# Kernel optimization log

Measured on AMD Instinct MI355X. Metric: run time of the kernel, lower is better.

The kernel has to match this reference:

```python
import jax, jax.numpy as jnp
import numpy as np

N = 50000          # nodes
E = 1_600_000      # edges (avg degree 32)
IN_DIM = 1024
HID = 32           # int(sqrt(IN_DIM))
OUT_DIMS = (2, 3)  # multi-task classifier heads


def setup_inputs() -> dict:
    key = jax.random.key(0)
    ks = jax.random.split(key, 16)
    x = jax.random.normal(ks[0], (N, IN_DIM), dtype=jnp.float32)
    adj_rows = jax.random.randint(ks[1], (E,), 0, N, dtype=jnp.int32)
    adj_cols = jax.random.randint(ks[2], (E,), 0, N, dtype=jnp.int32)
    adj_vals = jax.random.uniform(ks[3], (E,), dtype=jnp.float32) / 32.0  # ~normalized adj

    def xn(k, fan_in, fan_out, gain=0.75):  # xavier_normal with gain 3/4 (selu_xn)
        std = gain * np.sqrt(2.0 / (fan_in + fan_out))
        return jax.random.normal(k, (fan_in, fan_out), dtype=jnp.float32) * std

    w1 = xn(ks[4], IN_DIM, HID)
    w2 = xn(ks[5], HID, HID)
    w3 = xn(ks[6], HID, HID)
    b1 = jnp.zeros((HID,), jnp.float32)
    b2 = jnp.zeros((HID,), jnp.float32)
    b3 = jnp.zeros((HID,), jnp.float32)
    # clf heads: nn.Linear(HID, num_class), xavier_normal gain 1, zero bias
    clf_w0 = xn(ks[7], HID, OUT_DIMS[0], gain=1.0).T  # stored torch-style [out, in]
    clf_w1 = xn(ks[8], HID, OUT_DIMS[1], gain=1.0).T
    clf_b0 = jnp.zeros((OUT_DIMS[0],), jnp.float32)
    clf_b1 = jnp.zeros((OUT_DIMS[1],), jnp.float32)
    return {"x": x, "adj_rows": adj_rows, "adj_cols": adj_cols, "adj_vals": adj_vals,
            "w1": w1, "b1": b1, "w2": w2, "b2": b2, "w3": w3, "b3": b3,
            "clf_w0": clf_w0, "clf_b0": clf_b0, "clf_w1": clf_w1, "clf_b1": clf_b1}


def reference(x, adj_rows, adj_cols, adj_vals, w1, b1, w2, b2, w3, b3,
              clf_w0, clf_b0, clf_w1, clf_b1):
    def gcn_layer(h, w, b):
        support = h @ w                                   # [N, out]
        msgs = adj_vals[:, None] * support[adj_cols]      # gather along edges
        agg = jax.ops.segment_sum(msgs, adj_rows, num_segments=N)  # SpMM
        # eval mode: UniformDropout is identity; then SELU, then bias add
        return jax.nn.selu(agg) + b

    h = gcn_layer(x, w1, b1)
    h = gcn_layer(h, w2, b2)
    h = gcn_layer(h, w3, b3)
    out0 = h @ clf_w0.T + clf_b0   # [N, 2]
    out1 = h @ clf_w1.T + clf_b1   # [N, 3]
    return (out0, out1)
```

## Files before the change

### kernel.cpp

```cpp
#include <hip/hip_runtime.h>

#define IN_DIM 1024
#define HID 32
#define BSHIFT 5
#define BROWS 32
#define MAXB 1600
#define NBLK 128
#define SORT_CAP 4096

typedef _Float16 h4 __attribute__((ext_vector_type(4)));

__device__ __forceinline__ float4 h4_to_f4(h4 v) {
    float4 r;
    r.x = (float)v.x; r.y = (float)v.y; r.z = (float)v.z; r.w = (float)v.w;
    return r;
}

__device__ __forceinline__ float selu_f(float x) {
    const float scale = 1.0507009873554805f;
    const float alpha = 1.6732632423543772f;
    return x > 0.f ? scale * x : scale * alpha * (expf(x) - 1.f);
}


__global__ __launch_bounds__(1024) void part_hist(const int* __restrict__ rows, int E, int NB,
                                                  int nchunk, int* __restrict__ counts) {
    __shared__ int lh[MAXB];
    int tid = threadIdx.x, blk = blockIdx.x;
    for (int b = tid; b < NB; b += 1024) lh[b] = 0;
    __syncthreads();
    int base = blk * nchunk;
    int end = base + nchunk; if (end > E) end = E;
    for (int i = base + tid; i < end; i += 1024)
        atomicAdd(&lh[rows[i] >> BSHIFT], 1);
    __syncthreads();
    for (int b = tid; b < NB; b += 1024) counts[blk * NB + b] = lh[b];
}

__global__ __launch_bounds__(1024) void scan1_kernel(const int* __restrict__ counts, int M,
                                                     int NB,
                                                     int* __restrict__ offs,
                                                     int* __restrict__ partials) {
    __shared__ int s[1024];
    int tid = threadIdx.x;
    int i = blockIdx.x * 1024 + tid;
    int v = 0;
    if (i < M) {
        int b = i >> 7;
        int blk = i & (NBLK - 1);
        v = counts[blk * NB + b];
    }
    s[tid] = v;
    __syncthreads();
    for (int off = 1; off < 1024; off <<= 1) {
        int t = (tid >= off) ? s[tid - off] : 0;
        __syncthreads();
        s[tid] += t;
        __syncthreads();
    }
    if (i < M) offs[i] = s[tid] - v;
    if (tid == 1023) partials[blockIdx.x] = s[tid];
}

__global__ __launch_bounds__(1024) void scan_fix_kernel(int* __restrict__ offs,
                                                        const int* __restrict__ partials,
                                                        int M, int nb1) {
    __shared__ int s[256];
    int tid = threadIdx.x;
    if (tid < 256) s[tid] = (tid < nb1) ? partials[tid] : 0;
    __syncthreads();
    for (int off = 1; off < 256; off <<= 1) {
        int t = 0;
        if (tid < 256 && tid >= off) t = s[tid - off];
        __syncthreads();
        if (tid < 256) s[tid] += t;
        __syncthreads();
    }
    int myoff = (blockIdx.x == 0) ? 0 : s[blockIdx.x - 1];
    int i = blockIdx.x * 1024 + tid;
    if (i < M) offs[i] += myoff;
}

__global__ __launch_bounds__(1024) void part_scatter(const int* __restrict__ rows,
                                                     const int* __restrict__ cols,
                                                     const float* __restrict__ vals, int E,
                                                     int NB, int nchunk,
                                                     const int* __restrict__ offs,
                                                     int2* __restrict__ edata) {
    __shared__ int lc[MAXB];
    int tid = threadIdx.x, blk = blockIdx.x;
    for (int b = tid; b < NB; b += 1024) lc[b] = offs[b * NBLK + blk];
    __syncthreads();
    int base = blk * nchunk;
    int end = base + nchunk; if (end > E) end = E;
    for (int i = base + tid; i < end; i += 1024) {
        int r = rows[i];
        int b = r >> BSHIFT;
        int p = atomicAdd(&lc[b], 1);
        int2 pr;
        pr.x = ((r & (BROWS - 1)) << 18) | cols[i];
        pr.y = __float_as_int(vals[i]);
        edata[p] = pr;
    }
}

__global__ __launch_bounds__(256) void bucket_sort(int2* __restrict__ edata,
                                                   const int* __restrict__ offs,
                                                   int E, int NB,
                                                   int* __restrict__ rowptr) {
    __shared__ int2 stage[SORT_CAP];
    __shared__ int cnt[32], startsh[32], cur[32];
    int b = blockIdx.x, tid = threadIdx.x;
    int s0 = offs[b * NBLK];
    int s1 = (b + 1 < NB) ? offs[(b + 1) * NBLK] : E;
    int n = s1 - s0;
    if (tid < 32) cnt[tid] = 0;
    __syncthreads();
    for (int i = tid; i < n; i += 256) {
        int2 pr = edata[s0 + i];
        stage[i] = pr;
        atomicAdd(&cnt[pr.x >> 18], 1);
    }
    __syncthreads();
    if (tid == 0) {
        int run = 0;
        #pragma unroll
        for (int k = 0; k < 32; ++k) { startsh[k] = run; run += cnt[k]; }
    }
    __syncthreads();
    if (tid < 32) {
        cur[tid] = startsh[tid];
        rowptr[b * BROWS + tid] = s0 + startsh[tid];
    }
    __syncthreads();
    for (int i = tid; i < n; i += 256) {
        int2 pr = stage[i];
        int p = atomicAdd(&cur[pr.x >> 18], 1);
        edata[s0 + p] = pr;
    }
}


#define BR 128
#define BK 64
#define XS_LD (BK + 4)

__global__ __launch_bounds__(256) void gemm1_kernel(const float* __restrict__ x,
                                                    const float* __restrict__ w,
                                                    _Float16* __restrict__ out, int N) {
    __shared__ float xs[BR * XS_LD];
    __shared__ float ws[BK * HID];
    int tid = threadIdx.x;
    int ct = tid & 7;
    int d0 = ct * 4;
    int rt = tid >> 3;
    int row0 = blockIdx.x * BR;

    float4 acc0 = {0,0,0,0}, acc1 = {0,0,0,0}, acc2 = {0,0,0,0}, acc3 = {0,0,0,0};

    for (int kc = 0; kc < IN_DIM; kc += BK) {
        #pragma unroll
        for (int j = 0; j < 8; ++j) {
            int linear = tid + j * 256;
            int rr = linear >> 4;
            int cc = linear & 15;
            int grow = row0 + rr;
            if (grow > N - 1) grow = N - 1;
            float4 t = *(const float4*)&x[(size_t)grow * IN_DIM + kc + cc * 4];
            *(float4*)&xs[rr * XS_LD + cc * 4] = t;
        }
        #pragma unroll
        for (int j = 0; j < 2; ++j) {
            int linear = tid + j * 256;
            int kk = linear >> 3;
            int dd = (linear & 7) * 4;
            float4 t = *(const float4*)&w[(kc + kk) * HID + dd];
            *(float4*)&ws[kk * HID + dd] = t;
        }
        __syncthreads();
        #pragma unroll
        for (int k4 = 0; k4 < BK / 4; ++k4) {
            float4 wv0 = *(const float4*)&ws[(k4 * 4 + 0) * HID + d0];
            float4 wv1 = *(const float4*)&ws[(k4 * 4 + 1) * HID + d0];
            float4 wv2 = *(const float4*)&ws[(k4 * 4 + 2) * HID + d0];
            float4 wv3 = *(const float4*)&ws[(k4 * 4 + 3) * HID + d0];
            float4 xv;
            #define GEMM_STEP(ACC, I) \
                xv = *(const float4*)&xs[(rt + 32 * I) * XS_LD + k4 * 4]; \
                ACC.x += xv.x * wv0.x; ACC.y += xv.x * wv0.y; ACC.z += xv.x * wv0.z; ACC.w += xv.x * wv0.w; \
                ACC.x += xv.y * wv1.x; ACC.y += xv.y * wv1.y; ACC.z += xv.y * wv1.z; ACC.w += xv.y * wv1.w; \
                ACC.x += xv.z * wv2.x; ACC.y += xv.z * wv2.y; ACC.z += xv.z * wv2.z; ACC.w += xv.z * wv2.w; \
                ACC.x += xv.w * wv3.x; ACC.y += xv.w * wv3.y; ACC.z += xv.w * wv3.z; ACC.w += xv.w * wv3.w;
            GEMM_STEP(acc0, 0)
            GEMM_STEP(acc1, 1)
            GEMM_STEP(acc2, 2)
            GEMM_STEP(acc3, 3)
            #undef GEMM_STEP
        }
        __syncthreads();
    }
    {
        int grow = row0 + rt;
        h4 o;
        o.x = (_Float16)acc0.x; o.y = (_Float16)acc0.y; o.z = (_Float16)acc0.z; o.w = (_Float16)acc0.w;
        if (grow < N)       *(h4*)&out[(size_t)grow * HID + d0] = o;
        grow += 32;
        o.x = (_Float16)acc1.x; o.y = (_Float16)acc1.y; o.z = (_Float16)acc1.z; o.w = (_Float16)acc1.w;
        if (grow < N)       *(h4*)&out[(size_t)grow * HID + d0] = o;
        grow += 32;
        o.x = (_Float16)acc2.x; o.y = (_Float16)acc2.y; o.z = (_Float16)acc2.z; o.w = (_Float16)acc2.w;
        if (grow < N)       *(h4*)&out[(size_t)grow * HID + d0] = o;
        grow += 32;
        o.x = (_Float16)acc3.x; o.y = (_Float16)acc3.y; o.z = (_Float16)acc3.z; o.w = (_Float16)acc3.w;
        if (grow < N)       *(h4*)&out[(size_t)grow * HID + d0] = o;
    }
}


__device__ __forceinline__ float4 spmm_row_f4(const h4* __restrict__ sup,
                                              const int2* __restrict__ edata,
                                              int e0, int e1, int l) {
    float4 a0 = {0.f,0.f,0.f,0.f}, a1 = a0, a2 = a0, a3 = a0;
    int e = e0;
    for (; e + 8 <= e1; e += 8) {
        int2 m0 = edata[e],   m1 = edata[e+1], m2 = edata[e+2], m3 = edata[e+3];
        int2 m4 = edata[e+4], m5 = edata[e+5], m6 = edata[e+6], m7 = edata[e+7];
        h4 g0 = sup[(size_t)(m0.x & 0x3FFFF) * 8 + l];
        h4 g1 = sup[(size_t)(m1.x & 0x3FFFF) * 8 + l];
        h4 g2 = sup[(size_t)(m2.x & 0x3FFFF) * 8 + l];
        h4 g3 = sup[(size_t)(m3.x & 0x3FFFF) * 8 + l];
        h4 g4 = sup[(size_t)(m4.x & 0x3FFFF) * 8 + l];
        h4 g5 = sup[(size_t)(m5.x & 0x3FFFF) * 8 + l];
        h4 g6 = sup[(size_t)(m6.x & 0x3FFFF) * 8 + l];
        h4 g7 = sup[(size_t)(m7.x & 0x3FFFF) * 8 + l];
        float v0 = __int_as_float(m0.y), v1 = __int_as_float(m1.y);
        float v2 = __int_as_float(m2.y), v3 = __int_as_float(m3.y);
        float v4 = __int_as_float(m4.y), v5 = __int_as_float(m5.y);
        float v6 = __int_as_float(m6.y), v7 = __int_as_float(m7.y);
        float4 f0 = h4_to_f4(g0), f1 = h4_to_f4(g1), f2 = h4_to_f4(g2), f3 = h4_to_f4(g3);
        float4 f4_ = h4_to_f4(g4), f5 = h4_to_f4(g5), f6 = h4_to_f4(g6), f7 = h4_to_f4(g7);
        a0.x += v0*f0.x; a0.y += v0*f0.y; a0.z += v0*f0.z; a0.w += v0*f0.w;
        a1.x += v1*f1.x; a1.y += v1*f1.y; a1.z += v1*f1.z; a1.w += v1*f1.w;
        a2.x += v2*f2.x; a2.y += v2*f2.y; a2.z += v2*f2.z; a2.w += v2*f2.w;
        a3.x += v3*f3.x; a3.y += v3*f3.y; a3.z += v3*f3.z; a3.w += v3*f3.w;
        a0.x += v4*f4_.x; a0.y += v4*f4_.y; a0.z += v4*f4_.z; a0.w += v4*f4_.w;
        a1.x += v5*f5.x; a1.y += v5*f5.y; a1.z += v5*f5.z; a1.w += v5*f5.w;
        a2.x += v6*f6.x; a2.y += v6*f6.y; a2.z += v6*f6.z; a2.w += v6*f6.w;
        a3.x += v7*f7.x; a3.y += v7*f7.y; a3.z += v7*f7.z; a3.w += v7*f7.w;
    }
    for (; e < e1; ++e) {
        int2 m0 = edata[e];
        h4 g0 = sup[(size_t)(m0.x & 0x3FFFF) * 8 + l];
        float v0 = __int_as_float(m0.y);
        float4 f0 = h4_to_f4(g0);
        a0.x += v0*f0.x; a0.y += v0*f0.y; a0.z += v0*f0.z; a0.w += v0*f0.w;
    }
    a0.x += a1.x + a2.x + a3.x;
    a0.y += a1.y + a2.y + a3.y;
    a0.z += a1.z + a2.z + a3.z;
    a0.w += a1.w + a2.w + a3.w;
    return a0;
}

__global__ __launch_bounds__(256) void spmm_mid_kernel(const h4* __restrict__ sup,
                                                       const int* __restrict__ rowptr,
                                                       const int2* __restrict__ edata,
                                                       int N,
                                                       const float* __restrict__ bias,
                                                       const float* __restrict__ Wn,
                                                       _Float16* __restrict__ out) {
    __shared__ float Wsh[HID * HID];
    __shared__ float hs[BROWS][36];
    int tid = threadIdx.x;
    int b = blockIdx.x;
    *(float4*)&Wsh[tid * 4] = ((const float4*)Wn)[tid];
    int g = tid >> 3, l = tid & 7;
    int row = b * BROWS + g;
    float4 acc = {0.f,0.f,0.f,0.f};
    if (row < N) {
        int e0 = rowptr[row];
        int e1 = rowptr[row + 1];
        acc = spmm_row_f4(sup, edata, e0, e1, l);
    }
    float4 b4 = ((const float4*)bias)[l];
    float4 h;
    h.x = selu_f(acc.x) + b4.x;
    h.y = selu_f(acc.y) + b4.y;
    h.z = selu_f(acc.z) + b4.z;
    h.w = selu_f(acc.w) + b4.w;
    *(float4*)&hs[g][l * 4] = h;
    __syncthreads();
    int d = tid & 31;
    #pragma unroll
    for (int k = 0; k < 4; ++k) {
        int rl = (tid >> 5) + k * 8;
        int rrow = b * BROWS + rl;
        float o = 0.f;
        #pragma unroll
        for (int j = 0; j < HID; ++j) o += hs[rl][j] * Wsh[j * HID + d];
        if (rrow < N) out[(size_t)rrow * HID + d] = (_Float16)o;
    }
}

__global__ __launch_bounds__(256) void spmm_final_kernel(const h4* __restrict__ sup,
                                                         const int* __restrict__ rowptr,
                                                         const int2* __restrict__ edata,
                                                         int N,
                                                         const float* __restrict__ bias,
                                                         const float* __restrict__ cw0,
                                                         const float* __restrict__ cb0,
                                                         const float* __restrict__ cw1,
                                                         const float* __restrict__ cb1,
                                                         float* __restrict__ out) {
    __shared__ float hs[BROWS][36];
    int tid = threadIdx.x;
    int b = blockIdx.x;
    int g = tid >> 3, l = tid & 7;
    int row = b * BROWS + g;
    float4 acc = {0.f,0.f,0.f,0.f};
    if (row < N) {
        int e0 = rowptr[row];
        int e1 = rowptr[row + 1];
        acc = spmm_row_f4(sup, edata, e0, e1, l);
    }
    float4 b4 = ((const float4*)bias)[l];
    float4 h;
    h.x = selu_f(acc.x) + b4.x;
    h.y = selu_f(acc.y) + b4.y;
    h.z = selu_f(acc.z) + b4.z;
    h.w = selu_f(acc.w) + b4.w;
    *(float4*)&hs[g][l * 4] = h;
    __syncthreads();
    if (tid < BROWS * 5) {
        int rl = tid / 5, t = tid % 5;
        int rrow = b * BROWS + rl;
        if (rrow < N) {
            if (t < 2) {
                float o = cb0[t];
                #pragma unroll
                for (int j = 0; j < HID; ++j) o += hs[rl][j] * cw0[t * HID + j];
                out[(size_t)rrow * 2 + t] = o;
            } else {
                int c = t - 2;
                float o = cb1[c];
                #pragma unroll
                for (int j = 0; j < HID; ++j) o += hs[rl][j] * cw1[c * HID + j];
                out[(size_t)N * 2 + (size_t)rrow * 3 + c] = o;
            }
        }
    }
}


extern "C" void kernel_launch(void* const* d_in, const int* in_sizes, int n_in,
                              void* d_out, int out_size, void* d_ws, size_t ws_size,
                              hipStream_t stream) {
    const float* x        = (const float*)d_in[0];
    const int*   adj_rows = (const int*)d_in[1];
    const int*   adj_cols = (const int*)d_in[2];
    const float* adj_vals = (const float*)d_in[3];
    const float* w1 = (const float*)d_in[4];
    const float* b1 = (const float*)d_in[5];
    const float* w2 = (const float*)d_in[6];
    const float* b2 = (const float*)d_in[7];
    const float* w3 = (const float*)d_in[8];
    const float* b3 = (const float*)d_in[9];
    const float* cw0 = (const float*)d_in[10];
    const float* cb0 = (const float*)d_in[11];
    const float* cw1 = (const float*)d_in[12];
    const float* cb1 = (const float*)d_in[13];

    int N = in_sizes[0] / IN_DIM;
    int E = in_sizes[1];
    int NB = (N + BROWS - 1) >> BSHIFT;
    int M = NB * NBLK;
    int nchunk = (E + NBLK - 1) / NBLK;
    int nb1 = (M + 1023) / 1024;

    char* p = (char*)d_ws;
    _Float16* s_a = (_Float16*)p; p += (size_t)N * HID * sizeof(float);
    _Float16* s_b = (_Float16*)p; p += (size_t)N * HID * sizeof(float);
    int2*  edata = (int2*)p;  p += (size_t)E * sizeof(int2);
    int*   counts   = (int*)p; p += (size_t)M * sizeof(int);
    int*   offs     = (int*)p; p += (size_t)M * sizeof(int);
    int*   rowptr   = (int*)p; p += (size_t)(NB * BROWS + 1) * sizeof(int);
    int*   partials = (int*)p; p += 256 * sizeof(int);

    part_hist<<<NBLK, 1024, 0, stream>>>(adj_rows, E, NB, nchunk, counts);
    scan1_kernel<<<nb1, 1024, 0, stream>>>(counts, M, NB, offs, partials);
    scan_fix_kernel<<<nb1, 1024, 0, stream>>>(offs, partials, M, nb1);
    part_scatter<<<NBLK, 1024, 0, stream>>>(adj_rows, adj_cols, adj_vals, E, NB, nchunk,
                                            offs, edata);
    bucket_sort<<<NB, 256, 0, stream>>>(edata, offs, E, NB, rowptr);

    gemm1_kernel<<<(N + BR - 1) / BR, 256, 0, stream>>>(x, w1, s_a, N);
    spmm_mid_kernel<<<NB, 256, 0, stream>>>((const h4*)s_a, rowptr, edata, N, b1, w2, s_b);
    spmm_mid_kernel<<<NB, 256, 0, stream>>>((const h4*)s_b, rowptr, edata, N, b2, w3, s_a);
    spmm_final_kernel<<<NB, 256, 0, stream>>>((const h4*)s_a, rowptr, edata, N,
                                              b3, cw0, cb0, cw1, cb1, (float*)d_out);
}
```

Baseline: 461.1 us.

## Fuse edge partitioning, scan and bucket sort into one grid-barrier kernel

Replaces the five separate preprocessing kernels (histogram, two-level scan, scatter, per-bucket sort) with a single persistent kernel of 192 blocks. The stages are separated by a software grid barrier built on an atomic counter. The goal is to remove inter-kernel launch gaps and the separate scan-fix pass. The trade-offs are that correctness depends on all blocks being co-resident, a memset is added to reset the barrier, and the bucket sort now loops over buckets with 192 blocks instead of launching one block per bucket.

```diff
diff --git a/kernel.cpp b/kernel.cpp
--- a/kernel.cpp
+++ b/kernel.cpp
@@ -5,7 +5,8 @@
 #define BSHIFT 5
 #define BROWS 32
 #define MAXB 1600
-#define NBLK 128
+#define NBLKP 192
+#define PTHREADS 512
 #define SORT_CAP 4096
 
 typedef _Float16 h4 __attribute__((ext_vector_type(4)));
@@ -22,121 +23,157 @@
     return x > 0.f ? scale * x : scale * alpha * (expf(x) - 1.f);
 }
 
-
-__global__ __launch_bounds__(1024) void part_hist(const int* __restrict__ rows, int E, int NB,
-                                                  int nchunk, int* __restrict__ counts) {
-    __shared__ int lh[MAXB];
-    int tid = threadIdx.x, blk = blockIdx.x;
-    for (int b = tid; b < NB; b += 1024) lh[b] = 0;
+__device__ __forceinline__ void gridbar(int* bar, int phase) {
     __syncthreads();
-    int base = blk * nchunk;
-    int end = base + nchunk; if (end > E) end = E;
-    for (int i = base + tid; i < end; i += 1024)
-        atomicAdd(&lh[rows[i] >> BSHIFT], 1);
+    if (threadIdx.x == 0) {
+        __threadfence();
+        atomicAdd(bar, 1);
+        int target = phase * NBLKP;
+        int guard = 0;
+        while (atomicAdd(bar, 0) < target) {
+            __builtin_amdgcn_s_sleep(8);
+            if (++guard > (1 << 24)) break;
+        }
+        __threadfence();
+    }
     __syncthreads();
-    for (int b = tid; b < NB; b += 1024) counts[blk * NB + b] = lh[b];
-}
-
-__global__ __launch_bounds__(1024) void scan1_kernel(const int* __restrict__ counts, int M,
-                                                     int NB,
-                                                     int* __restrict__ offs,
-                                                     int* __restrict__ partials) {
-    __shared__ int s[1024];
-    int tid = threadIdx.x;
-    int i = blockIdx.x * 1024 + tid;
-    int v = 0;
-    if (i < M) {
-        int b = i >> 7;
-        int blk = i & (NBLK - 1);
-        v = counts[blk * NB + b];
-    }
-    s[tid] = v;
-    __syncthreads();
-    for (int off = 1; off < 1024; off <<= 1) {
-        int t = (tid >= off) ? s[tid - off] : 0;
-        __syncthreads();
-        s[tid] += t;
-        __syncthreads();
-    }
-    if (i < M) offs[i] = s[tid] - v;
-    if (tid == 1023) partials[blockIdx.x] = s[tid];
-}
-
-__global__ __launch_bounds__(1024) void scan_fix_kernel(int* __restrict__ offs,
-                                                        const int* __restrict__ partials,
-                                                        int M, int nb1) {
-    __shared__ int s[256];
-    int tid = threadIdx.x;
-    if (tid < 256) s[tid] = (tid < nb1) ? partials[tid] : 0;
-    __syncthreads();
-    for (int off = 1; off < 256; off <<= 1) {
-        int t = 0;
-        if (tid < 256 && tid >= off) t = s[tid - off];
-        __syncthreads();
-        if (tid < 256) s[tid] += t;
-        __syncthreads();
-    }
-    int myoff = (blockIdx.x == 0) ? 0 : s[blockIdx.x - 1];
-    int i = blockIdx.x * 1024 + tid;
-    if (i < M) offs[i] += myoff;
-}
-
-__global__ __launch_bounds__(1024) void part_scatter(const int* __restrict__ rows,
-                                                     const int* __restrict__ cols,
-                                                     const float* __restrict__ vals, int E,
-                                                     int NB, int nchunk,
-                                                     const int* __restrict__ offs,
-                                                     int2* __restrict__ edata) {
-    __shared__ int lc[MAXB];
-    int tid = threadIdx.x, blk = blockIdx.x;
-    for (int b = tid; b < NB; b += 1024) lc[b] = offs[b * NBLK + blk];
-    __syncthreads();
-    int base = blk * nchunk;
-    int end = base + nchunk; if (end > E) end = E;
-    for (int i = base + tid; i < end; i += 1024) {
-        int r = rows[i];
-        int b = r >> BSHIFT;
-        int p = atomicAdd(&lc[b], 1);
-        int2 pr;
-        pr.x = ((r & (BROWS - 1)) << 18) | cols[i];
-        pr.y = __float_as_int(vals[i]);
-        edata[p] = pr;
-    }
-}
-
-__global__ __launch_bounds__(256) void bucket_sort(int2* __restrict__ edata,
-                                                   const int* __restrict__ offs,
-                                                   int E, int NB,
-                                                   int* __restrict__ rowptr) {
-    __shared__ int2 stage[SORT_CAP];
-    __shared__ int cnt[32], startsh[32], cur[32];
-    int b = blockIdx.x, tid = threadIdx.x;
-    int s0 = offs[b * NBLK];
-    int s1 = (b + 1 < NB) ? offs[(b + 1) * NBLK] : E;
-    int n = s1 - s0;
-    if (tid < 32) cnt[tid] = 0;
-    __syncthreads();
-    for (int i = tid; i < n; i += 256) {
-        int2 pr = edata[s0 + i];
-        stage[i] = pr;
-        atomicAdd(&cnt[pr.x >> 18], 1);
-    }
-    __syncthreads();
-    if (tid == 0) {
-        int run = 0;
+}
+
+
+__global__ __launch_bounds__(PTHREADS) void prep_kernel(
+        const int* __restrict__ rows, const int* __restrict__ cols,
+        const float* __restrict__ vals, int E, int N, int NB,
+        int* __restrict__ counts,
+        int* __restrict__ offs,
+        int* __restrict__ partials,
+        int* __restrict__ bar,
+        int2* __restrict__ edata,
+        int* __restrict__ rowptr) {
+    __shared__ alignas(16) char smem_raw[SORT_CAP * sizeof(int2) + 4096];
+    int tid = threadIdx.x, bid = blockIdx.x;
+    int M = NB * NBLKP;
+    int ECH = (E + NBLKP - 1) / NBLKP;
+    int e0 = bid * ECH;
+    int e1 = e0 + ECH; if (e1 > E) e1 = E;
+
+    {
+        int* lh = (int*)smem_raw;
+        for (int b = tid; b < NB; b += PTHREADS) lh[b] = 0;
+        __syncthreads();
+        for (int i = e0 + tid; i < e1; i += PTHREADS)
+            atomicAdd(&lh[rows[i] >> BSHIFT], 1);
+        __syncthreads();
+        for (int b = tid; b < NB; b += PTHREADS) counts[b * NBLKP + bid] = lh[b];
+    }
+    gridbar(bar, 1);
+
+    int CHM = (M + NBLKP - 1) / NBLKP;
+    int base = bid * CHM;
+    int loc[4];
+    int run = 0;
+    #pragma unroll
+    for (int j = 0; j < 4; ++j) {
+        int li = tid * 4 + j;
+        int idx = base + li;
+        loc[j] = (li < CHM && idx < M) ? counts[idx] : 0;
+        run += loc[j];
+    }
+    int excl;
+    {
+        int* s = (int*)smem_raw;
+        s[tid] = run;
+        __syncthreads();
+        for (int off = 1; off < PTHREADS; off <<= 1) {
+            int t = (tid >= off) ? s[tid - off] : 0;
+            __syncthreads();
+            s[tid] += t;
+            __syncthreads();
+        }
+        excl = s[tid] - run;
+        if (tid == PTHREADS - 1) atomicExch(&partials[bid], s[tid]);
+    }
+    gridbar(bar, 2);
+
+    if (bid == 0) {
+        int* sp = (int*)smem_raw + PTHREADS;
+        int own = 0;
+        if (tid < NBLKP) own = atomicAdd(&partials[tid], 0);
+        if (tid < 256) sp[tid] = (tid < NBLKP) ? own : 0;
+        __syncthreads();
+        for (int off = 1; off < 256; off <<= 1) {
+            int t = (tid < 256 && tid >= off) ? sp[tid - off] : 0;
+            __syncthreads();
+            if (tid < 256) sp[tid] += t;
+            __syncthreads();
+        }
+        if (tid < NBLKP) atomicExch(&partials[tid], sp[tid] - own);
+    }
+    gridbar(bar, 3);
+
+    {
+        int blkoff = atomicAdd(&partials[bid], 0);
+        int running = blkoff + excl;
         #pragma unroll
-        for (int k = 0; k < 32; ++k) { startsh[k] = run; run += cnt[k]; }
-    }
-    __syncthreads();
-    if (tid < 32) {
-        cur[tid] = startsh[tid];
-        rowptr[b * BROWS + tid] = s0 + startsh[tid];
-    }
-    __syncthreads();
-    for (int i = tid; i < n; i += 256) {
-        int2 pr = stage[i];
-        int p = atomicAdd(&cur[pr.x >> 18], 1);
-        edata[s0 + p] = pr;
+        for (int j = 0; j < 4; ++j) {
+            int li = tid * 4 + j;
+            int idx = base + li;
+            if (li < CHM && idx < M) offs[idx] = running;
+            running += loc[j];
+        }
+    }
+    gridbar(bar, 4);
+
+    {
+        int* lc = (int*)smem_raw;
+        for (int b = tid; b < NB; b += PTHREADS) lc[b] = offs[b * NBLKP + bid];
+        __syncthreads();
+        for (int i = e0 + tid; i < e1; i += PTHREADS) {
+            int r = rows[i];
+            int b = r >> BSHIFT;
+            int p = atomicAdd(&lc[b], 1);
+            int2 pr;
+            pr.x = ((r & (BROWS - 1)) << 18) | cols[i];
+            pr.y = __float_as_int(vals[i]);
+            edata[p] = pr;
+        }
+    }
+    gridbar(bar, 5);
+
+    {
+        int2* stage  = (int2*)smem_raw;
+        int* cnt32   = (int*)(smem_raw + SORT_CAP * sizeof(int2));
+        int* start32 = cnt32 + 32;
+        int* cur32   = cnt32 + 64;
+        for (int bk = bid; bk < NB; bk += NBLKP) {
+            int s0 = offs[bk * NBLKP];
+            int s1 = (bk + 1 < NB) ? offs[(bk + 1) * NBLKP] : E;
+            int n = s1 - s0;
+            if (tid < 32) cnt32[tid] = 0;
+            __syncthreads();
+            for (int i = tid; i < n; i += PTHREADS) {
+                int2 pr = edata[s0 + i];
+                stage[i] = pr;
+                atomicAdd(&cnt32[pr.x >> 18], 1);
+            }
+            __syncthreads();
+            if (tid == 0) {
+                int runb = 0;
+                #pragma unroll
+                for (int k = 0; k < 32; ++k) { start32[k] = runb; runb += cnt32[k]; }
+            }
+            __syncthreads();
+            if (tid < 32) {
+                cur32[tid] = start32[tid];
+                rowptr[bk * BROWS + tid] = s0 + start32[tid];
+            }
+            __syncthreads();
+            for (int i = tid; i < n; i += PTHREADS) {
+                int2 pr = stage[i];
+                int p = atomicAdd(&cur32[pr.x >> 18], 1);
+                edata[s0 + p] = pr;
+            }
+            __syncthreads();
+        }
     }
 }
 
@@ -373,9 +410,7 @@
     int N = in_sizes[0] / IN_DIM;
     int E = in_sizes[1];
     int NB = (N + BROWS - 1) >> BSHIFT;
-    int M = NB * NBLK;
-    int nchunk = (E + NBLK - 1) / NBLK;
-    int nb1 = (M + 1023) / 1024;
+    int M = NB * NBLKP;
 
     char* p = (char*)d_ws;
     _Float16* s_a = (_Float16*)p; p += (size_t)N * HID * sizeof(float);
@@ -385,13 +420,12 @@
     int*   offs     = (int*)p; p += (size_t)M * sizeof(int);
     int*   rowptr   = (int*)p; p += (size_t)(NB * BROWS + 1) * sizeof(int);
     int*   partials = (int*)p; p += 256 * sizeof(int);
-
-    part_hist<<<NBLK, 1024, 0, stream>>>(adj_rows, E, NB, nchunk, counts);
-    scan1_kernel<<<nb1, 1024, 0, stream>>>(counts, M, NB, offs, partials);
-    scan_fix_kernel<<<nb1, 1024, 0, stream>>>(offs, partials, M, nb1);
-    part_scatter<<<NBLK, 1024, 0, stream>>>(adj_rows, adj_cols, adj_vals, E, NB, nchunk,
-                                            offs, edata);
-    bucket_sort<<<NB, 256, 0, stream>>>(edata, offs, E, NB, rowptr);
+    int*   bar      = (int*)p; p += 64;
+
+    hipMemsetAsync(bar, 0, 64, stream);
+
+    prep_kernel<<<NBLKP, PTHREADS, 0, stream>>>(adj_rows, adj_cols, adj_vals, E, N, NB,
+                                                counts, offs, partials, bar, edata, rowptr);
 
     gemm1_kernel<<<(N + BR - 1) / BR, 256, 0, stream>>>(x, w1, s_a, N);
     spmm_mid_kernel<<<NB, 256, 0, stream>>>((const h4*)s_a, rowptr, edata, N, b1, w2, s_b);
```

After: 543.7 us. 17.9% more time.

## Replace scan-based edge partition with fixed-capacity padded buckets via global atomics

Applied to the files above, without the earlier changes.

Fuses the histogram, two-level scan and scatter kernels into a single kernel. It reserves per-bucket slots with global atomics into fixed-capacity padded buckets (1536 edges per 32-row bucket). The bucket sort and SpMM kernels then read from padded storage using int2 (start,end) row ranges. This removes several kernel launches and the global prefix-scan passes. The cost is extra memory, and edges are silently dropped if any bucket exceeds the capacity, so it only works for near-uniform degree distributions.

```diff
diff --git a/kernel.cpp b/kernel.cpp
--- a/kernel.cpp
+++ b/kernel.cpp
@@ -5,8 +5,8 @@
 #define BSHIFT 5
 #define BROWS 32
 #define MAXB 1600
-#define NBLK 128
-#define SORT_CAP 4096
+#define NBLKS 256
+#define CAP 1536
 
 typedef _Float16 h4 __attribute__((ext_vector_type(4)));
 
@@ -23,9 +23,14 @@
 }
 
 
-__global__ __launch_bounds__(1024) void part_hist(const int* __restrict__ rows, int E, int NB,
-                                                  int nchunk, int* __restrict__ counts) {
+__global__ __launch_bounds__(1024) void scatter_pad(const int* __restrict__ rows,
+                                                    const int* __restrict__ cols,
+                                                    const float* __restrict__ vals,
+                                                    int E, int NB, int nchunk,
+                                                    int* __restrict__ bcnt,
+                                                    int2* __restrict__ epad) {
     __shared__ int lh[MAXB];
+    __shared__ int lc[MAXB];
     int tid = threadIdx.x, blk = blockIdx.x;
     for (int b = tid; b < NB; b += 1024) lh[b] = 0;
     __syncthreads();
@@ -34,90 +39,38 @@
     for (int i = base + tid; i < end; i += 1024)
         atomicAdd(&lh[rows[i] >> BSHIFT], 1);
     __syncthreads();
-    for (int b = tid; b < NB; b += 1024) counts[blk * NB + b] = lh[b];
-}
-
-__global__ __launch_bounds__(1024) void scan1_kernel(const int* __restrict__ counts, int M,
-                                                     int NB,
-                                                     int* __restrict__ offs,
-                                                     int* __restrict__ partials) {
-    __shared__ int s[1024];
-    int tid = threadIdx.x;
-    int i = blockIdx.x * 1024 + tid;
-    int v = 0;
-    if (i < M) {
-        int b = i >> 7;
-        int blk = i & (NBLK - 1);
-        v = counts[blk * NB + b];
-    }
-    s[tid] = v;
-    __syncthreads();
-    for (int off = 1; off < 1024; off <<= 1) {
-        int t = (tid >= off) ? s[tid - off] : 0;
-        __syncthreads();
-        s[tid] += t;
-        __syncthreads();
-    }
-    if (i < M) offs[i] = s[tid] - v;
-    if (tid == 1023) partials[blockIdx.x] = s[tid];
-}
-
-__global__ __launch_bounds__(1024) void scan_fix_kernel(int* __restrict__ offs,
-                                                        const int* __restrict__ partials,
-                                                        int M, int nb1) {
-    __shared__ int s[256];
-    int tid = threadIdx.x;
-    if (tid < 256) s[tid] = (tid < nb1) ? partials[tid] : 0;
-    __syncthreads();
-    for (int off = 1; off < 256; off <<= 1) {
-        int t = 0;
-        if (tid < 256 && tid >= off) t = s[tid - off];
-        __syncthreads();
-        if (tid < 256) s[tid] += t;
-        __syncthreads();
-    }
-    int myoff = (blockIdx.x == 0) ? 0 : s[blockIdx.x - 1];
-    int i = blockIdx.x * 1024 + tid;
-    if (i < M) offs[i] += myoff;
-}
-
-__global__ __launch_bounds__(1024) void part_scatter(const int* __restrict__ rows,
-                                                     const int* __restrict__ cols,
-                                                     const float* __restrict__ vals, int E,
-                                                     int NB, int nchunk,
-                                                     const int* __restrict__ offs,
-                                                     int2* __restrict__ edata) {
-    __shared__ int lc[MAXB];
-    int tid = threadIdx.x, blk = blockIdx.x;
-    for (int b = tid; b < NB; b += 1024) lc[b] = offs[b * NBLK + blk];
-    __syncthreads();
-    int base = blk * nchunk;
-    int end = base + nchunk; if (end > E) end = E;
+    for (int b = tid; b < NB; b += 1024) {
+        int c = lh[b];
+        lc[b] = (c > 0) ? atomicAdd(&bcnt[b], c) : 0;
+    }
+    __syncthreads();
     for (int i = base + tid; i < end; i += 1024) {
         int r = rows[i];
         int b = r >> BSHIFT;
         int p = atomicAdd(&lc[b], 1);
-        int2 pr;
-        pr.x = ((r & (BROWS - 1)) << 18) | cols[i];
-        pr.y = __float_as_int(vals[i]);
-        edata[p] = pr;
-    }
-}
-
-__global__ __launch_bounds__(256) void bucket_sort(int2* __restrict__ edata,
-                                                   const int* __restrict__ offs,
-                                                   int E, int NB,
-                                                   int* __restrict__ rowptr) {
-    __shared__ int2 stage[SORT_CAP];
+        if (p < CAP) {
+            int2 pr;
+            pr.x = ((r & (BROWS - 1)) << 18) | cols[i];
+            pr.y = __float_as_int(vals[i]);
+            epad[(size_t)b * CAP + p] = pr;
+        }
+    }
+}
+
+
+__global__ __launch_bounds__(256) void sort_pad(int2* __restrict__ epad,
+                                                const int* __restrict__ bcnt,
+                                                int NB,
+                                                int2* __restrict__ rowptr2) {
+    __shared__ int2 stage[CAP];
     __shared__ int cnt[32], startsh[32], cur[32];
     int b = blockIdx.x, tid = threadIdx.x;
-    int s0 = offs[b * NBLK];
-    int s1 = (b + 1 < NB) ? offs[(b + 1) * NBLK] : E;
-    int n = s1 - s0;
+    int n = bcnt[b]; if (n > CAP) n = CAP;
+    int s0 = b * CAP;
     if (tid < 32) cnt[tid] = 0;
     __syncthreads();
     for (int i = tid; i < n; i += 256) {
-        int2 pr = edata[s0 + i];
+        int2 pr = epad[s0 + i];
         stage[i] = pr;
         atomicAdd(&cnt[pr.x >> 18], 1);
     }
@@ -130,13 +83,14 @@
     __syncthreads();
     if (tid < 32) {
         cur[tid] = startsh[tid];
-        rowptr[b * BROWS + tid] = s0 + startsh[tid];
+        rowptr2[b * BROWS + tid] = make_int2(s0 + startsh[tid],
+                                             s0 + startsh[tid] + cnt[tid]);
     }
     __syncthreads();
     for (int i = tid; i < n; i += 256) {
         int2 pr = stage[i];
         int p = atomicAdd(&cur[pr.x >> 18], 1);
-        edata[s0 + p] = pr;
+        epad[s0 + p] = pr;
     }
 }
 
@@ -263,7 +217,7 @@
 }
 
 __global__ __launch_bounds__(256) void spmm_mid_kernel(const h4* __restrict__ sup,
-                                                       const int* __restrict__ rowptr,
+                                                       const int2* __restrict__ rowptr2,
                                                        const int2* __restrict__ edata,
                                                        int N,
                                                        const float* __restrict__ bias,
@@ -278,9 +232,8 @@
     int row = b * BROWS + g;
     float4 acc = {0.f,0.f,0.f,0.f};
     if (row < N) {
-        int e0 = rowptr[row];
-        int e1 = rowptr[row + 1];
-        acc = spmm_row_f4(sup, edata, e0, e1, l);
+        int2 ee = rowptr2[row];
+        acc = spmm_row_f4(sup, edata, ee.x, ee.y, l);
     }
     float4 b4 = ((const float4*)bias)[l];
     float4 h;
@@ -303,7 +256,7 @@
 }
 
 __global__ __launch_bounds__(256) void spmm_final_kernel(const h4* __restrict__ sup,
-                                                         const int* __restrict__ rowptr,
+                                                         const int2* __restrict__ rowptr2,
                                                          const int2* __restrict__ edata,
                                                          int N,
                                                          const float* __restrict__ bias,
@@ -319,9 +272,8 @@
     int row = b * BROWS + g;
     float4 acc = {0.f,0.f,0.f,0.f};
     if (row < N) {
-        int e0 = rowptr[row];
-        int e1 = rowptr[row + 1];
-        acc = spmm_row_f4(sup, edata, e0, e1, l);
+        int2 ee = rowptr2[row];
+        acc = spmm_row_f4(sup, edata, ee.x, ee.y, l);
     }
     float4 b4 = ((const float4*)bias)[l];
     float4 h;
@@ -373,29 +325,24 @@
     int N = in_sizes[0] / IN_DIM;
     int E = in_sizes[1];
     int NB = (N + BROWS - 1) >> BSHIFT;
-    int M = NB * NBLK;
-    int nchunk = (E + NBLK - 1) / NBLK;
-    int nb1 = (M + 1023) / 1024;
+    int nchunk = (E + NBLKS - 1) / NBLKS;
 
     char* p = (char*)d_ws;
     _Float16* s_a = (_Float16*)p; p += (size_t)N * HID * sizeof(float);
     _Float16* s_b = (_Float16*)p; p += (size_t)N * HID * sizeof(float);
-    int2*  edata = (int2*)p;  p += (size_t)E * sizeof(int2);
-    int*   counts   = (int*)p; p += (size_t)M * sizeof(int);
-    int*   offs     = (int*)p; p += (size_t)M * sizeof(int);
-    int*   rowptr   = (int*)p; p += (size_t)(NB * BROWS + 1) * sizeof(int);
-    int*   partials = (int*)p; p += 256 * sizeof(int);
-
-    part_hist<<<NBLK, 1024, 0, stream>>>(adj_rows, E, NB, nchunk, counts);
-    scan1_kernel<<<nb1, 1024, 0, stream>>>(counts, M, NB, offs, partials);
-    scan_fix_kernel<<<nb1, 1024, 0, stream>>>(offs, partials, M, nb1);
-    part_scatter<<<NBLK, 1024, 0, stream>>>(adj_rows, adj_cols, adj_vals, E, NB, nchunk,
-                                            offs, edata);
-    bucket_sort<<<NB, 256, 0, stream>>>(edata, offs, E, NB, rowptr);
+    int2*  epad    = (int2*)p; p += (size_t)NB * CAP * sizeof(int2);
+    int*   bcnt    = (int*)p;  p += (size_t)NB * sizeof(int);
+    int2*  rowptr2 = (int2*)p; p += (size_t)NB * BROWS * sizeof(int2);
+
+    hipMemsetAsync(bcnt, 0, (size_t)NB * sizeof(int), stream);
+
+    scatter_pad<<<NBLKS, 1024, 0, stream>>>(adj_rows, adj_cols, adj_vals, E, NB, nchunk,
+                                            bcnt, epad);
+    sort_pad<<<NB, 256, 0, stream>>>(epad, bcnt, NB, rowptr2);
 
     gemm1_kernel<<<(N + BR - 1) / BR, 256, 0, stream>>>(x, w1, s_a, N);
-    spmm_mid_kernel<<<NB, 256, 0, stream>>>((const h4*)s_a, rowptr, edata, N, b1, w2, s_b);
-    spmm_mid_kernel<<<NB, 256, 0, stream>>>((const h4*)s_b, rowptr, edata, N, b2, w3, s_a);
-    spmm_final_kernel<<<NB, 256, 0, stream>>>((const h4*)s_a, rowptr, edata, N,
+    spmm_mid_kernel<<<NB, 256, 0, stream>>>((const h4*)s_a, rowptr2, epad, N, b1, w2, s_b);
+    spmm_mid_kernel<<<NB, 256, 0, stream>>>((const h4*)s_b, rowptr2, epad, N, b2, w3, s_a);
+    spmm_final_kernel<<<NB, 256, 0, stream>>>((const h4*)s_a, rowptr2, epad, N,
                                               b3, cw0, cb0, cw1, cb1, (float*)d_out);
 }
```

Result: faster. 441.7 us (-4.2%).
